# Kernel optimization log

Measured on AMD Instinct MI355X. Metric: run time of the kernel, lower is better.

## Reference

```python
import jax, jax.numpy as jnp
import numpy as np

B, SEG, DIM = 8, 16, 1024  # H = W = D = SEG is forced by the Linear(dim, dim) on H*S etc.
HID = DIM // 4


def setup_inputs() -> dict:
    key = jax.random.key(0)
    ks = jax.random.split(key, 16)
    def lin(k, i, o):
        return jax.random.normal(k, (i, o), jnp.float32) * 0.02
    return {
        "x": jax.random.normal(ks[0], (B, SEG, SEG, SEG, DIM), jnp.float32),
        "wh": lin(ks[1], DIM, DIM), "bh": jnp.zeros((DIM,), jnp.float32),
        "ww": lin(ks[2], DIM, DIM), "bw": jnp.zeros((DIM,), jnp.float32),
        "wd": lin(ks[3], DIM, DIM), "bd": jnp.zeros((DIM,), jnp.float32),
        "wc": lin(ks[4], DIM, DIM), "bc": jnp.zeros((DIM,), jnp.float32),
        "w1": lin(ks[5], DIM, HID), "b1": jnp.zeros((HID,), jnp.float32),
        "w2": lin(ks[6], HID, 4 * DIM), "b2": jnp.zeros((4 * DIM,), jnp.float32),
        "wp": lin(ks[7], DIM, DIM), "bp": jnp.zeros((DIM,), jnp.float32),
    }


def reference(x, wh, bh, ww, bw, wd, bd, wc, bc, w1, b1, w2, b2, wp, bp):
    Bn, H, Wn, D, C = x.shape
    seg = SEG
    S = C // seg
    xr = x.reshape(Bn, H, Wn, D, seg, S)

    # h-branch: mix along H axis (H*S == C)
    h = xr.transpose(0, 4, 2, 3, 1, 5).reshape(Bn, seg, Wn, D, H * S)
    h = (h @ wh + bh).reshape(Bn, seg, Wn, D, H, S).transpose(0, 4, 2, 3, 1, 5).reshape(Bn, H, Wn, D, C)

    # w-branch: mix along W axis
    w = xr.transpose(0, 1, 4, 3, 2, 5).reshape(Bn, H, seg, D, Wn * S)
    w = (w @ ww + bw).reshape(Bn, H, seg, D, Wn, S).transpose(0, 1, 4, 3, 2, 5).reshape(Bn, H, Wn, D, C)

    # d-branch: mix along D axis
    d = xr.transpose(0, 1, 2, 4, 3, 5).reshape(Bn, H, Wn, seg, D * S)
    d = (d @ wd + bd).reshape(Bn, H, Wn, seg, D, S).transpose(0, 1, 2, 4, 3, 5).reshape(Bn, H, Wn, D, C)

    # c-branch: plain channel mixing
    c = x @ wc + bc

    # reweight gate: global-average-pool then small MLP -> softmax over the 4 branches
    a = (h + w + d + c).mean(axis=(1, 2, 3))                 # (B, C)
    a = jax.nn.gelu(a @ w1 + b1, approximate=False) @ w2 + b2  # (B, 4C)
    a = jax.nn.softmax(a.reshape(Bn, C, 4).transpose(2, 0, 1), axis=0)  # (4, B, C)
    a = a[:, :, None, None, None, :]                          # (4, B, 1, 1, 1, C)

    out = h * a[0] + w * a[1] + d * a[2] + c * a[3]
    return out @ wp + bp
```

## Files before the change

### kernel.cpp

```cpp
#include <hip/hip_runtime.h>
#include <cstdint>
#include <cstddef>

typedef unsigned short u16;
typedef __attribute__((ext_vector_type(8))) __bf16 bf16x8;
typedef __attribute__((ext_vector_type(4))) float f32x4;
typedef __attribute__((ext_vector_type(4))) unsigned int u32x4;

__device__ __forceinline__ float bf2f(u16 u){
  union { unsigned int i; float f; } x; x.i = ((unsigned int)u) << 16; return x.f;
}
__device__ __forceinline__ u16 f2bf(float f){
  union { float f; unsigned int i; } x; x.f = f;
  unsigned int i = x.i;
  return (u16)((i + 0x7fffu + ((i >> 16) & 1u)) >> 16);
}
__device__ __forceinline__ void load_lds16(const u16* g, u16* l){
  __builtin_amdgcn_global_load_lds((const __attribute__((address_space(1))) void*)g,
                                   (__attribute__((address_space(3))) void*)l, 16, 0, 0);
}

__global__ __launch_bounds__(256) void k_transpose(
    const float* __restrict__ wh, const float* __restrict__ ww,
    const float* __restrict__ wd, const float* __restrict__ wc,
    const float* __restrict__ wp, u16* __restrict__ wT)
{
  __shared__ u16 tile[32][33];
  const float* src = (blockIdx.z==0)?wh:(blockIdx.z==1)?ww:(blockIdx.z==2)?wd:(blockIdx.z==3)?wc:wp;
  u16* dst = wT + (size_t)blockIdx.z * 1048576;
  int x = blockIdx.x*32 + threadIdx.x;
  int y0 = blockIdx.y*32;
  for (int i = threadIdx.y; i < 32; i += 8)
    tile[i][threadIdx.x] = f2bf(src[(size_t)(y0+i)*1024 + x]);
  __syncthreads();
  int x2 = y0 + threadIdx.x;
  int y2 = blockIdx.x*32;
  for (int i = threadIdx.y; i < 32; i += 8)
    dst[(size_t)(y2+i)*1024 + x2] = tile[threadIdx.x][i];
}

__global__ __launch_bounds__(256) void k_cast(const float* __restrict__ x, u16* __restrict__ xbf)
{
  size_t i = (size_t)blockIdx.x*256 + threadIdx.x;
  const f32x4* p = (const f32x4*)(x + i*8);
  f32x4 a = p[0], b = p[1];
  union { u32x4 v; u16 u[8]; } o;
#pragma unroll
  for (int e = 0; e < 4; ++e){ o.u[e] = f2bf(a[e]); o.u[e+4] = f2bf(b[e]); }
  *(u32x4*)(xbf + i*8) = o.v;
}

__global__ __launch_bounds__(256) void k_psum(
    const float* __restrict__ x, float* __restrict__ P_h,
    float* __restrict__ PwP, float* __restrict__ PdP)
{
  const int b = blockIdx.x, cs = blockIdx.y, hg = blockIdx.z;
  const int th = threadIdx.x >> 7, tc = threadIdx.x & 127;
  const int h = hg*2 + th, c = cs*128 + tc;
  const float* xb = x + ((size_t)b<<22) + ((size_t)h<<18) + c;
  float sh = 0.f;
  float aW[16] = {}, aD[16] = {};
#pragma unroll
  for (int w = 0; w < 16; ++w)
#pragma unroll
    for (int d = 0; d < 16; ++d){
      float v = xb[(w<<14) + (d<<10)];
      sh += v; aW[w] += v; aD[d] += v;
    }
  P_h[(size_t)((b<<4)+h)*1024 + c] = sh;
  const int part = hg*2 + th;
  float* pw = PwP + ((size_t)part<<17) + ((size_t)b<<14) + c;
  float* pd = PdP + ((size_t)part<<17) + ((size_t)b<<14) + c;
#pragma unroll
  for (int w = 0; w < 16; ++w) pw[w<<10] = aW[w];
#pragma unroll
  for (int d = 0; d < 16; ++d) pd[d<<10] = aD[d];
}

__global__ __launch_bounds__(256) void k_psum2(
    const float* __restrict__ PwP, const float* __restrict__ PdP,
    float* __restrict__ P_w, float* __restrict__ P_d)
{
  int idx = blockIdx.x*256 + threadIdx.x;
  float s = 0.f, t = 0.f;
#pragma unroll
  for (int p = 0; p < 16; ++p){ s += PwP[(size_t)p*131072 + idx]; t += PdP[(size_t)p*131072 + idx]; }
  P_w[idx] = s; P_d[idx] = t;
}

__global__ __launch_bounds__(256) void k_wred(
    const float* __restrict__ wh, const float* __restrict__ ww, const float* __restrict__ wd,
    float* __restrict__ wred)
{
  const float* src = (blockIdx.y==0)?wh:(blockIdx.y==1)?ww:wd;
  int idx = blockIdx.x*256 + threadIdx.x;
  int k = idx >> 6, S = idx & 63;
  float s = 0.f;
#pragma unroll
  for (int i = 0; i < 16; ++i) s += src[(size_t)k*1024 + i*64 + S];
  wred[(size_t)blockIdx.y*65536 + idx] = s;
}

__global__ __launch_bounds__(128) void k_asum(
    const float* __restrict__ P_h, const float* __restrict__ P_w, const float* __restrict__ P_d,
    const float* __restrict__ wred, const float* __restrict__ wc,
    const float* __restrict__ bhv, const float* __restrict__ bwv,
    const float* __restrict__ bdv, const float* __restrict__ bcv,
    float* __restrict__ a_sum)
{
  const int b = blockIdx.x, cs = blockIdx.y, tid = threadIdx.x;
  const int c = cs*128 + tid, sg = c >> 6, S = c & 63;
  __shared__ float xbar[1024];
  for (int k = tid; k < 1024; k += 128){
    float s = 0.f;
#pragma unroll
    for (int hh = 0; hh < 16; ++hh) s += P_h[(size_t)(b*16+hh)*1024 + k];
    xbar[k] = s;
  }
  __syncthreads();
  const float* Ph = P_h + (size_t)b*16384;
  const float* Pw = P_w + (size_t)b*16384;
  const float* Pd = P_d + (size_t)b*16384;
  const float* whr = wred, *wwr = wred + 65536, *wdr = wred + 131072;
  float bs = 0.f;
#pragma unroll
  for (int i = 0; i < 16; ++i) bs += bhv[i*64+S] + bwv[i*64+S] + bdv[i*64+S];
  float acc = 4096.f * bcv[c] + 256.f * bs;
  for (int i = 0; i < 16; ++i){
#pragma unroll 8
    for (int si = 0; si < 64; ++si){
      int k = i*64 + si;
      acc += Ph[i*1024 + sg*64 + si] * whr[(size_t)k*64 + S]
           + Pw[i*1024 + sg*64 + si] * wwr[(size_t)k*64 + S]
           + Pd[i*1024 + sg*64 + si] * wdr[(size_t)k*64 + S];
    }
  }
#pragma unroll 8
  for (int k = 0; k < 1024; ++k) acc += xbar[k] * wc[(size_t)k*1024 + c];
  a_sum[b*1024 + c] = acc;
}

__global__ __launch_bounds__(256) void k_mlp1(
    const float* __restrict__ a_sum, const float* __restrict__ w1,
    const float* __restrict__ b1, float* __restrict__ z1g)
{
  const int b = blockIdx.x, tid = threadIdx.x;
  __shared__ float af[1024];
  for (int i = tid; i < 1024; i += 256) af[i] = a_sum[b*1024 + i] * (1.0f/4096.0f);
  __syncthreads();
  float acc = b1[tid];
#pragma unroll 8
  for (int k = 0; k < 1024; ++k) acc += af[k] * w1[(size_t)k*256 + tid];
  z1g[b*256 + tid] = 0.5f * acc * (1.0f + erff(acc * 0.70710678118654752f));
}

__global__ __launch_bounds__(128) void k_mlp2(
    const float* __restrict__ z1g, const float* __restrict__ w2,
    const float* __restrict__ b2, float* __restrict__ alpha)
{
  const int b = blockIdx.x, js = blockIdx.y, tid = threadIdx.x;
  __shared__ float z1[256];
  z1[tid] = z1g[b*256 + tid];
  z1[tid+128] = z1g[b*256 + tid + 128];
  __syncthreads();
  const int cch = js*128 + tid;
  const int j0 = cch*4;
  f32x4 acc = *(const f32x4*)(b2 + j0);
#pragma unroll 8
  for (int k = 0; k < 256; ++k){
    f32x4 wv4 = *(const f32x4*)(w2 + (size_t)k*4096 + j0);
    float z = z1[k];
    acc[0] += z*wv4[0]; acc[1] += z*wv4[1]; acc[2] += z*wv4[2]; acc[3] += z*wv4[3];
  }
  float m = fmaxf(fmaxf(acc[0], acc[1]), fmaxf(acc[2], acc[3]));
  float e0 = expf(acc[0]-m), e1 = expf(acc[1]-m), e2 = expf(acc[2]-m), e3 = expf(acc[3]-m);
  float inv = 1.0f / (e0+e1+e2+e3);
  alpha[0*8192 + b*1024 + cch] = e0*inv;
  alpha[1*8192 + b*1024 + cch] = e1*inv;
  alpha[2*8192 + b*1024 + cch] = e2*inv;
  alpha[3*8192 + b*1024 + cch] = e3*inv;
}

__global__ __launch_bounds__(256) void k_branch_gemm(
    const u16* __restrict__ xbf, const u16* __restrict__ wT,
    const float* __restrict__ bh, const float* __restrict__ bw,
    const float* __restrict__ bd, const float* __restrict__ bc,
    u16* __restrict__ hbuf, u16* __restrict__ wbuf,
    u16* __restrict__ dbuf, u16* __restrict__ cbuf)
{
  const int branch = blockIdx.z;
  const int ntile  = blockIdx.x;
  const int rtile  = blockIdx.y;
  const int tid = threadIdx.x;
  const int wv = tid >> 6, l = tid & 63;

  __shared__ __align__(16) u16 As[4096];
  __shared__ __align__(16) u16 Bs[4096];

  const u16* wsel = wT + (size_t)branch * 1048576;
  const float* bias = (branch==0)?bh:(branch==1)?bw:(branch==2)?bd:bc;
  u16* obuf         = (branch==0)?hbuf:(branch==1)?wbuf:(branch==2)?dbuf:cbuf;

  const int srow0 = wv*32 + (l>>2);
  const int kelem = (l & 3) * 8;
  size_t basea0, basea1; int strideK;
  {
    int r  = rtile*128 + srow0;
    int r2 = r + 16;
    int b0=r>>12,  q1=(r>>8)&15,  q2=(r>>4)&15,  q3=r&15;
    int b1_=r2>>12, p1=(r2>>8)&15, p2=(r2>>4)&15, p3=r2&15;
    if      (branch==0){ basea0=((size_t)b0<<22)+(q2<<14)+(q3<<10)+(q1<<6);
                         basea1=((size_t)b1_<<22)+(p2<<14)+(p3<<10)+(p1<<6); strideK=262144; }
    else if (branch==1){ basea0=((size_t)b0<<22)+((size_t)q1<<18)+(q3<<10)+(q2<<6);
                         basea1=((size_t)b1_<<22)+((size_t)p1<<18)+(p3<<10)+(p2<<6); strideK=16384; }
    else if (branch==2){ basea0=((size_t)b0<<22)+((size_t)q1<<18)+(q2<<14)+(q3<<6);
                         basea1=((size_t)b1_<<22)+((size_t)p1<<18)+(p2<<14)+(p3<<6); strideK=1024; }
    else               { basea0=(size_t)r<<10; basea1=(size_t)r2<<10; strideK=64; }
  }
  const u16* ga0 = xbf + basea0 + kelem;
  const u16* ga1 = xbf + basea1 + kelem;
  const u16* bp0 = wsel + (size_t)(ntile*128 + srow0)*1024 + kelem;
  const u16* bp1 = bp0 + 16*1024;
  u16* lA0 = As + wv*1024;        u16* lA1 = As + wv*1024 + 512;
  u16* lB0 = Bs + wv*1024;        u16* lB1 = Bs + wv*1024 + 512;

  const int wm = wv >> 1, wn = wv & 1;
  const int fr = l & 15, fq = (l >> 4) * 8;
  const u16* ard = As + (wm*64 + fr)*32 + fq;
  const u16* brd = Bs + (wn*64 + fr)*32 + fq;
  f32x4 acc[4][4] = {};

  for (int s = 0; s < 32; ++s){
    size_t koff = (size_t)(s>>1)*strideK + (size_t)(s&1)*32;
    load_lds16(ga0 + koff, lA0);
    load_lds16(ga1 + koff, lA1);
    load_lds16(bp0 + s*32, lB0);
    load_lds16(bp1 + s*32, lB1);
    __syncthreads();
    bf16x8 af[4], bf[4];
#pragma unroll
    for (int i = 0; i < 4; ++i){
      af[i] = *(const bf16x8*)(ard + i*16*32);
      bf[i] = *(const bf16x8*)(brd + i*16*32);
    }
#pragma unroll
    for (int mf = 0; mf < 4; ++mf)
#pragma unroll
      for (int nf = 0; nf < 4; ++nf)
        acc[mf][nf] = __builtin_amdgcn_mfma_f32_16x16x32_bf16(af[mf], bf[nf], acc[mf][nf], 0, 0, 0);
    __syncthreads();
  }

#pragma unroll
  for (int mf = 0; mf < 4; ++mf)
#pragma unroll
    for (int nf = 0; nf < 4; ++nf){
      int col = ntile*128 + wn*64 + nf*16 + fr;
      float bv = bias[col];
      int row0 = rtile*128 + wm*64 + mf*16 + (l>>4)*4;
#pragma unroll
      for (int rg = 0; rg < 4; ++rg)
        obuf[(size_t)(row0+rg)*1024 + col] = f2bf(acc[mf][nf][rg] + bv);
    }
}

__global__ __launch_bounds__(256) void k_mix(
    const u16* __restrict__ hbuf, const u16* __restrict__ wbuf,
    const u16* __restrict__ dbuf, const u16* __restrict__ cbuf,
    u16* __restrict__ mix, const float* __restrict__ alpha)
{
  int idx = blockIdx.x*256 + threadIdx.x;
  int p  = idx >> 7;
  int c0 = (idx & 127) << 3;
  int b = p >> 12, h = (p >> 8) & 15, w = (p >> 4) & 15, d = p & 15;
  int sg = c0 >> 6, s = c0 & 63;
  size_t bb = (size_t)b << 22;
  union { u32x4 v; u16 u[8]; } hv, wv, dv, cv, mv;
  hv.v = *(const u32x4*)(hbuf + bb + (sg<<18) + (w<<14) + (d<<10) + (h<<6) + s);
  wv.v = *(const u32x4*)(wbuf + bb + (h<<18) + (sg<<14) + (d<<10) + (w<<6) + s);
  dv.v = *(const u32x4*)(dbuf + bb + (h<<18) + (w<<14) + (sg<<10) + (d<<6) + s);
  cv.v = *(const u32x4*)(cbuf + ((size_t)p<<10) + c0);
  union { f32x4 f[2]; float a[8]; } a0, a1, a2, a3;
  const float* ab = alpha + b*1024 + c0;
  a0.f[0] = *(const f32x4*)(ab);         a0.f[1] = *(const f32x4*)(ab + 4);
  a1.f[0] = *(const f32x4*)(ab + 8192);  a1.f[1] = *(const f32x4*)(ab + 8196);
  a2.f[0] = *(const f32x4*)(ab + 16384); a2.f[1] = *(const f32x4*)(ab + 16388);
  a3.f[0] = *(const f32x4*)(ab + 24576); a3.f[1] = *(const f32x4*)(ab + 24580);
#pragma unroll
  for (int e = 0; e < 8; ++e){
    float m = a0.a[e]*bf2f(hv.u[e]) + a1.a[e]*bf2f(wv.u[e])
            + a2.a[e]*bf2f(dv.u[e]) + a3.a[e]*bf2f(cv.u[e]);
    mv.u[e] = f2bf(m);
  }
  *(u32x4*)(mix + ((size_t)p<<10) + c0) = mv.v;
}

__global__ __launch_bounds__(256) void k_final_gemm(
    const u16* __restrict__ A, const u16* __restrict__ wpT,
    const float* __restrict__ bp, float* __restrict__ out)
{
  const int ntile = blockIdx.x, rtile = blockIdx.y;
  const int tid = threadIdx.x;
  const int wv = tid >> 6, l = tid & 63;
  __shared__ __align__(16) u16 As[4096];
  __shared__ __align__(16) u16 Bs[4096];
  const int srow0 = wv*32 + (l>>2);
  const int kelem = (l & 3) * 8;
  const u16* ga0 = A + ((size_t)(rtile*128 + srow0) << 10) + kelem;
  const u16* ga1 = ga0 + (16 << 10);
  const u16* bp0 = wpT + (size_t)(ntile*128 + srow0)*1024 + kelem;
  const u16* bp1 = bp0 + 16*1024;
  u16* lA0 = As + wv*1024;        u16* lA1 = As + wv*1024 + 512;
  u16* lB0 = Bs + wv*1024;        u16* lB1 = Bs + wv*1024 + 512;
  const int wm = wv >> 1, wn = wv & 1;
  const int fr = l & 15, fq = (l >> 4) * 8;
  const u16* ard = As + (wm*64 + fr)*32 + fq;
  const u16* brd = Bs + (wn*64 + fr)*32 + fq;
  f32x4 acc[4][4] = {};

  for (int s = 0; s < 32; ++s){
    load_lds16(ga0 + s*32, lA0);
    load_lds16(ga1 + s*32, lA1);
    load_lds16(bp0 + s*32, lB0);
    load_lds16(bp1 + s*32, lB1);
    __syncthreads();
    bf16x8 af[4], bf[4];
#pragma unroll
    for (int i = 0; i < 4; ++i){
      af[i] = *(const bf16x8*)(ard + i*16*32);
      bf[i] = *(const bf16x8*)(brd + i*16*32);
    }
#pragma unroll
    for (int mf = 0; mf < 4; ++mf)
#pragma unroll
      for (int nf = 0; nf < 4; ++nf)
        acc[mf][nf] = __builtin_amdgcn_mfma_f32_16x16x32_bf16(af[mf], bf[nf], acc[mf][nf], 0, 0, 0);
    __syncthreads();
  }

#pragma unroll
  for (int mf = 0; mf < 4; ++mf)
#pragma unroll
    for (int nf = 0; nf < 4; ++nf){
      int col = ntile*128 + wn*64 + nf*16 + fr;
      float bv = bp[col];
      int row0 = rtile*128 + wm*64 + mf*16 + (l>>4)*4;
#pragma unroll
      for (int rg = 0; rg < 4; ++rg)
        out[(size_t)(row0+rg)*1024 + col] = acc[mf][nf][rg] + bv;
    }
}

extern "C" void kernel_launch(void* const* d_in, const int* in_sizes, int n_in,
                              void* d_out, int out_size, void* d_ws, size_t ws_size,
                              hipStream_t stream)
{
  const float* x  = (const float*)d_in[0];
  const float* wh = (const float*)d_in[1];
  const float* bh = (const float*)d_in[2];
  const float* ww = (const float*)d_in[3];
  const float* bw = (const float*)d_in[4];
  const float* wd = (const float*)d_in[5];
  const float* bd = (const float*)d_in[6];
  const float* wc = (const float*)d_in[7];
  const float* bc = (const float*)d_in[8];
  const float* w1 = (const float*)d_in[9];
  const float* b1 = (const float*)d_in[10];
  const float* w2 = (const float*)d_in[11];
  const float* b2 = (const float*)d_in[12];
  const float* wp = (const float*)d_in[13];
  const float* bp = (const float*)d_in[14];
  char* ws = (char*)d_ws;
  char* ob = (char*)d_out;

  u16*   xbf   = (u16*)(ws);
  u16*   hbuf  = (u16*)(ws + 67108864);
  u16*   wbuf  = (u16*)(ws + 134217728);
  u16*   wT    = (u16*)(ws + 201326592);
  float* a_sum = (float*)(ws + 211812352);
  float* alpha = (float*)(ws + 211845120);
  float* z1g   = (float*)(ws + 211976192);
  u16*   mixb  = xbf;

  float* PwP  = (float*)(ob);
  float* PdP  = (float*)(ob + 8388608);
  float* P_h  = (float*)(ob + 16777216);
  float* P_w  = (float*)(ob + 17301504);
  float* P_d  = (float*)(ob + 17825792);
  float* wred = (float*)(ob + 18350080);
  u16*   cbuf = (u16*)ob;
  u16*   dbuf = (u16*)(ob + 67108864);
  float* outp = (float*)d_out;

  k_transpose  <<<dim3(32, 32, 5), dim3(32, 8), 0, stream>>>(wh, ww, wd, wc, wp, wT);
  k_cast       <<<dim3(16384),     256, 0, stream>>>(x, xbf);
  k_psum       <<<dim3(8, 8, 8),   256, 0, stream>>>(x, P_h, PwP, PdP);
  k_psum2      <<<dim3(512),       256, 0, stream>>>(PwP, PdP, P_w, P_d);
  k_wred       <<<dim3(256, 3),    256, 0, stream>>>(wh, ww, wd, wred);
  k_asum       <<<dim3(8, 8),      128, 0, stream>>>(P_h, P_w, P_d, wred, wc, bh, bw, bd, bc, a_sum);
  k_mlp1       <<<dim3(8),         256, 0, stream>>>(a_sum, w1, b1, z1g);
  k_mlp2       <<<dim3(8, 8),      128, 0, stream>>>(z1g, w2, b2, alpha);
  k_branch_gemm<<<dim3(8, 256, 4), 256, 0, stream>>>(xbf, wT, bh, bw, bd, bc,
                                                     hbuf, wbuf, dbuf, cbuf);
  k_mix        <<<dim3(16384),     256, 0, stream>>>(hbuf, wbuf, dbuf, cbuf, mixb, alpha);
  k_final_gemm <<<dim3(8, 256),    256, 0, stream>>>(mixb, wT + 4*1048576, bp, outp);
  (void)in_sizes; (void)n_in; (void)out_size; (void)ws_size;
}
```

Before: 1.062 ms.

## Rewrite GEMMs as 256x256 pipelined tiles and fuse bf16 cast into psum

Both GEMM kernels now use 512-thread blocks computing 256x256 tiles. They use double-buffered LDS staging through direct global-to-LDS loads, an 8-phase interleaved schedule with explicit waitcnt, barriers and setprio, and an XCD-aware block-index swizzle. The goal is to hide load latency and raise MFMA utilisation. Separately, the standalone cast kernel is removed and the bf16 conversion is done inside k_psum, saving one full read of x. k_asum also splits its reduction across 256 threads for more parallelism. The larger tiles raise register and LDS pressure (128 KB of LDS per block).

```diff
diff --git a/kernel.cpp b/kernel.cpp
--- a/kernel.cpp
+++ b/kernel.cpp
@@ -39,25 +39,16 @@
     dst[(size_t)(y2+i)*1024 + x2] = tile[threadIdx.x][i];
 }
 
-__global__ __launch_bounds__(256) void k_cast(const float* __restrict__ x, u16* __restrict__ xbf)
-{
-  size_t i = (size_t)blockIdx.x*256 + threadIdx.x;
-  const f32x4* p = (const f32x4*)(x + i*8);
-  f32x4 a = p[0], b = p[1];
-  union { u32x4 v; u16 u[8]; } o;
-#pragma unroll
-  for (int e = 0; e < 4; ++e){ o.u[e] = f2bf(a[e]); o.u[e+4] = f2bf(b[e]); }
-  *(u32x4*)(xbf + i*8) = o.v;
-}
-
 __global__ __launch_bounds__(256) void k_psum(
-    const float* __restrict__ x, float* __restrict__ P_h,
+    const float* __restrict__ x, u16* __restrict__ xbf, float* __restrict__ P_h,
     float* __restrict__ PwP, float* __restrict__ PdP)
 {
   const int b = blockIdx.x, cs = blockIdx.y, hg = blockIdx.z;
   const int th = threadIdx.x >> 7, tc = threadIdx.x & 127;
   const int h = hg*2 + th, c = cs*128 + tc;
-  const float* xb = x + ((size_t)b<<22) + ((size_t)h<<18) + c;
+  const size_t base = ((size_t)b<<22) + ((size_t)h<<18) + c;
+  const float* xb = x + base;
+  u16* xo = xbf + base;
   float sh = 0.f;
   float aW[16] = {}, aD[16] = {};
 #pragma unroll
@@ -65,6 +56,7 @@
 #pragma unroll
     for (int d = 0; d < 16; ++d){
       float v = xb[(w<<14) + (d<<10)];
+      xo[(w<<14) + (d<<10)] = f2bf(v);
       sh += v; aW[w] += v; aD[d] += v;
     }
   P_h[(size_t)((b<<4)+h)*1024 + c] = sh;
@@ -101,7 +93,7 @@
   wred[(size_t)blockIdx.y*65536 + idx] = s;
 }
 
-__global__ __launch_bounds__(128) void k_asum(
+__global__ __launch_bounds__(256) void k_asum(
     const float* __restrict__ P_h, const float* __restrict__ P_w, const float* __restrict__ P_d,
     const float* __restrict__ wred, const float* __restrict__ wc,
     const float* __restrict__ bhv, const float* __restrict__ bwv,
@@ -109,9 +101,11 @@
     float* __restrict__ a_sum)
 {
   const int b = blockIdx.x, cs = blockIdx.y, tid = threadIdx.x;
-  const int c = cs*128 + tid, sg = c >> 6, S = c & 63;
+  const int tc = tid & 127, ti = tid >> 7;
+  const int c = cs*128 + tc, sg = c >> 6, S = c & 63;
   __shared__ float xbar[1024];
-  for (int k = tid; k < 1024; k += 128){
+  __shared__ float red[2][128];
+  for (int k = tid; k < 1024; k += 256){
     float s = 0.f;
 #pragma unroll
     for (int hh = 0; hh < 16; ++hh) s += P_h[(size_t)(b*16+hh)*1024 + k];
@@ -122,11 +116,8 @@
   const float* Pw = P_w + (size_t)b*16384;
   const float* Pd = P_d + (size_t)b*16384;
   const float* whr = wred, *wwr = wred + 65536, *wdr = wred + 131072;
-  float bs = 0.f;
-#pragma unroll
-  for (int i = 0; i < 16; ++i) bs += bhv[i*64+S] + bwv[i*64+S] + bdv[i*64+S];
-  float acc = 4096.f * bcv[c] + 256.f * bs;
-  for (int i = 0; i < 16; ++i){
+  float acc = 0.f;
+  for (int i = ti*8; i < ti*8 + 8; ++i){
 #pragma unroll 8
     for (int si = 0; si < 64; ++si){
       int k = i*64 + si;
@@ -136,8 +127,15 @@
     }
   }
 #pragma unroll 8
-  for (int k = 0; k < 1024; ++k) acc += xbar[k] * wc[(size_t)k*1024 + c];
-  a_sum[b*1024 + c] = acc;
+  for (int k = ti*512; k < ti*512 + 512; ++k) acc += xbar[k] * wc[(size_t)k*1024 + c];
+  red[ti][tc] = acc;
+  __syncthreads();
+  if (ti == 0){
+    float bs = 0.f;
+#pragma unroll
+    for (int i = 0; i < 16; ++i) bs += bhv[i*64+S] + bwv[i*64+S] + bdv[i*64+S];
+    a_sum[b*1024 + c] = red[0][tc] + red[1][tc] + 4096.f*bcv[c] + 256.f*bs;
+  }
 }
 
 __global__ __launch_bounds__(256) void k_mlp1(
@@ -181,86 +179,134 @@
   alpha[3*8192 + b*1024 + cch] = e3*inv;
 }
 
-__global__ __launch_bounds__(256) void k_branch_gemm(
+
+#define STAGE_A(buf, kk, kt) \
+  load_lds16(gA0 + (size_t)(kt)*strideK + (kk)*32, sA + (buf)*16384 + (kk)*8192); \
+  load_lds16(gA1 + (size_t)(kt)*strideK + (kk)*32, sA + (buf)*16384 + (kk)*8192 + 4096)
+#define STAGE_B(buf, kk, kt) \
+  load_lds16(gB0 + (kt)*64 + (kk)*32, sB + (buf)*16384 + (kk)*8192); \
+  load_lds16(gB1 + (kt)*64 + (kk)*32, sB + (buf)*16384 + (kk)*8192 + 4096)
+
+#define PHASE(h, kk, buf, STAGE_STMT, VM) do{ \
+  const u16* ar_ = ldsA + (buf)*16384 + (kk)*8192 + ardoff + (h)*2048; \
+  const u16* br_ = ldsB + (buf)*16384 + (kk)*8192 + brdoff; \
+  bf16x8 af_[4], bf_[4]; \
+  _Pragma("unroll") for (int m_ = 0; m_ < 4; ++m_) af_[m_] = *(const bf16x8*)(ar_ + m_*512); \
+  _Pragma("unroll") for (int n_ = 0; n_ < 4; ++n_) bf_[n_] = *(const bf16x8*)(br_ + n_*512); \
+  STAGE_STMT; \
+  if (VM) asm volatile("s_waitcnt vmcnt(4)" ::: "memory"); \
+  __builtin_amdgcn_s_barrier(); \
+  asm volatile("s_waitcnt lgkmcnt(0)" ::: "memory"); \
+  __builtin_amdgcn_sched_barrier(0); \
+  __builtin_amdgcn_s_setprio(1); \
+  _Pragma("unroll") for (int m_ = 0; m_ < 4; ++m_) \
+    _Pragma("unroll") for (int n_ = 0; n_ < 4; ++n_) \
+      acc[(h)*4+m_][n_] = __builtin_amdgcn_mfma_f32_16x16x32_bf16(af_[m_], bf_[n_], acc[(h)*4+m_][n_], 0, 0, 0); \
+  __builtin_amdgcn_s_setprio(0); \
+  __builtin_amdgcn_s_barrier(); \
+}while(0)
+
+#define GEMM_PROLOGUE() do{ \
+  load_lds16(gA0, sA);                 load_lds16(gA1, sA + 4096); \
+  load_lds16(gB0, sB);                 load_lds16(gB1, sB + 4096); \
+  load_lds16(gA0 + 32, sA + 8192);     load_lds16(gA1 + 32, sA + 8192 + 4096); \
+  load_lds16(gB0 + 32, sB + 8192);     load_lds16(gB1 + 32, sB + 8192 + 4096); \
+  load_lds16(gA0 + strideK, sA + 16384);   load_lds16(gA1 + strideK, sA + 16384 + 4096); \
+  load_lds16(gB0 + 64, sB + 16384);        load_lds16(gB1 + 64, sB + 16384 + 4096); \
+  asm volatile("s_waitcnt vmcnt(4)" ::: "memory"); \
+  __builtin_amdgcn_s_barrier(); \
+}while(0)
+
+#define GEMM_MAINLOOP() \
+  for (int i = 0; i < 8; ++i){ \
+    const int t1 = 2*i + 1; \
+    const int t2 = (2*i + 2 < 16) ? 2*i + 2 : 15; \
+    const int t3 = (2*i + 3 < 16) ? 2*i + 3 : 15; \
+    PHASE(0,0,0, STAGE_A(1,1,t1), 0); \
+    PHASE(1,0,0, STAGE_B(1,1,t1), 0); \
+    PHASE(0,1,0, STAGE_A(0,0,t2), 0); \
+    PHASE(1,1,0, STAGE_B(0,0,t2), 1); \
+    PHASE(0,0,1, STAGE_A(0,1,t2), 0); \
+    PHASE(1,0,1, STAGE_B(0,1,t2), 0); \
+    PHASE(0,1,1, STAGE_A(1,0,t3), 0); \
+    PHASE(1,1,1, STAGE_B(1,0,t3), 1); \
+  }
+
+__global__ __launch_bounds__(512, 2) void k_branch_gemm(
     const u16* __restrict__ xbf, const u16* __restrict__ wT,
     const float* __restrict__ bh, const float* __restrict__ bw,
     const float* __restrict__ bd, const float* __restrict__ bc,
     u16* __restrict__ hbuf, u16* __restrict__ wbuf,
     u16* __restrict__ dbuf, u16* __restrict__ cbuf)
 {
-  const int branch = blockIdx.z;
-  const int ntile  = blockIdx.x;
-  const int rtile  = blockIdx.y;
+  const int p = blockIdx.x;
+  const int id = (p & 7) * 256 + (p >> 3);
+  const int ntile  = id & 3;
+  const int rtile  = (id >> 2) & 127;
+  const int branch = id >> 9;
+
   const int tid = threadIdx.x;
   const int wv = tid >> 6, l = tid & 63;
 
-  __shared__ __align__(16) u16 As[4096];
-  __shared__ __align__(16) u16 Bs[4096];
+  __shared__ __align__(16) u16 ldsA[32768];
+  __shared__ __align__(16) u16 ldsB[32768];
 
   const u16* wsel = wT + (size_t)branch * 1048576;
   const float* bias = (branch==0)?bh:(branch==1)?bw:(branch==2)?bd:bc;
   u16* obuf         = (branch==0)?hbuf:(branch==1)?wbuf:(branch==2)?dbuf:cbuf;
 
-  const int srow0 = wv*32 + (l>>2);
-  const int kelem = (l & 3) * 8;
-  size_t basea0, basea1; int strideK;
+  const int lr = l >> 2;
+  const int qg = (l & 3) * 8;
+  int strideK;
+  size_t cb0, cb1;
   {
-    int r  = rtile*128 + srow0;
-    int r2 = r + 16;
-    int b0=r>>12,  q1=(r>>8)&15,  q2=(r>>4)&15,  q3=r&15;
-    int b1_=r2>>12, p1=(r2>>8)&15, p2=(r2>>4)&15, p3=r2&15;
-    if      (branch==0){ basea0=((size_t)b0<<22)+(q2<<14)+(q3<<10)+(q1<<6);
-                         basea1=((size_t)b1_<<22)+(p2<<14)+(p3<<10)+(p1<<6); strideK=262144; }
-    else if (branch==1){ basea0=((size_t)b0<<22)+((size_t)q1<<18)+(q3<<10)+(q2<<6);
-                         basea1=((size_t)b1_<<22)+((size_t)p1<<18)+(p3<<10)+(p2<<6); strideK=16384; }
-    else if (branch==2){ basea0=((size_t)b0<<22)+((size_t)q1<<18)+(q2<<14)+(q3<<6);
-                         basea1=((size_t)b1_<<22)+((size_t)p1<<18)+(p2<<14)+(p3<<6); strideK=1024; }
-    else               { basea0=(size_t)r<<10; basea1=(size_t)r2<<10; strideK=64; }
-  }
-  const u16* ga0 = xbf + basea0 + kelem;
-  const u16* ga1 = xbf + basea1 + kelem;
-  const u16* bp0 = wsel + (size_t)(ntile*128 + srow0)*1024 + kelem;
-  const u16* bp1 = bp0 + 16*1024;
-  u16* lA0 = As + wv*1024;        u16* lA1 = As + wv*1024 + 512;
-  u16* lB0 = Bs + wv*1024;        u16* lB1 = Bs + wv*1024 + 512;
-
-  const int wm = wv >> 1, wn = wv & 1;
-  const int fr = l & 15, fq = (l >> 4) * 8;
-  const u16* ard = As + (wm*64 + fr)*32 + fq;
-  const u16* brd = Bs + (wn*64 + fr)*32 + fq;
-  f32x4 acc[4][4] = {};
-
-  for (int s = 0; s < 32; ++s){
-    size_t koff = (size_t)(s>>1)*strideK + (size_t)(s&1)*32;
-    load_lds16(ga0 + koff, lA0);
-    load_lds16(ga1 + koff, lA1);
-    load_lds16(bp0 + s*32, lB0);
-    load_lds16(bp1 + s*32, lB1);
-    __syncthreads();
-    bf16x8 af[4], bf[4];
-#pragma unroll
-    for (int i = 0; i < 4; ++i){
-      af[i] = *(const bf16x8*)(ard + i*16*32);
-      bf[i] = *(const bf16x8*)(brd + i*16*32);
+    const int q1 = rtile & 15, b_ = rtile >> 4;
+    const size_t q2a = wv, q2b = wv + 8;
+    if (branch == 0){
+      cb0 = ((size_t)b_<<22) + (q2a<<14) + ((size_t)q1<<6);
+      cb1 = ((size_t)b_<<22) + (q2b<<14) + ((size_t)q1<<6);
+      strideK = 262144;
+    } else if (branch == 1){
+      cb0 = ((size_t)b_<<22) + ((size_t)q1<<18) + (q2a<<6);
+      cb1 = ((size_t)b_<<22) + ((size_t)q1<<18) + (q2b<<6);
+      strideK = 16384;
+    } else if (branch == 2){
+      cb0 = ((size_t)b_<<22) + ((size_t)q1<<18) + (q2a<<14);
+      cb1 = ((size_t)b_<<22) + ((size_t)q1<<18) + (q2b<<14);
+      strideK = 1024;
+    } else {
+      size_t r0 = (size_t)(rtile*256 + wv*16);
+      cb0 = r0 << 10; cb1 = (r0 + 128) << 10;
+      strideK = 64;
     }
-#pragma unroll
-    for (int mf = 0; mf < 4; ++mf)
-#pragma unroll
-      for (int nf = 0; nf < 4; ++nf)
-        acc[mf][nf] = __builtin_amdgcn_mfma_f32_16x16x32_bf16(af[mf], bf[nf], acc[mf][nf], 0, 0, 0);
-    __syncthreads();
-  }
-
-#pragma unroll
-  for (int mf = 0; mf < 4; ++mf)
+  }
+  const int rsh = (branch == 2) ? 6 : 10;
+  const u16* gA0 = xbf + cb0 + ((size_t)lr << rsh) + qg;
+  const u16* gA1 = xbf + cb1 + ((size_t)lr << rsh) + qg;
+  const u16* gB0 = wsel + (size_t)(ntile*256 + wv*16 + lr) * 1024 + qg;
+  const u16* gB1 = gB0 + 128*1024;
+  u16* sA = ldsA + wv*512;
+  u16* sB = ldsB + wv*512;
+
+  const int wm = wv >> 2, wn = wv & 3;
+  const int fr = l & 15;
+  const int ardoff = (wm*128 + fr)*32 + (l >> 4)*8;
+  const int brdoff = (wn*64  + fr)*32 + (l >> 4)*8;
+  f32x4 acc[8][4] = {};
+
+  GEMM_PROLOGUE();
+  GEMM_MAINLOOP();
+
+#pragma unroll
+  for (int mg = 0; mg < 8; ++mg)
 #pragma unroll
     for (int nf = 0; nf < 4; ++nf){
-      int col = ntile*128 + wn*64 + nf*16 + fr;
+      int col = ntile*256 + wn*64 + nf*16 + fr;
       float bv = bias[col];
-      int row0 = rtile*128 + wm*64 + mf*16 + (l>>4)*4;
+      int row0 = rtile*256 + wm*128 + mg*16 + (l>>4)*4;
 #pragma unroll
       for (int rg = 0; rg < 4; ++rg)
-        obuf[(size_t)(row0+rg)*1024 + col] = f2bf(acc[mf][nf][rg] + bv);
+        obuf[(size_t)(row0+rg)*1024 + col] = f2bf(acc[mg][nf][rg] + bv);
     }
 }
 
@@ -295,59 +341,51 @@
   *(u32x4*)(mix + ((size_t)p<<10) + c0) = mv.v;
 }
 
-__global__ __launch_bounds__(256) void k_final_gemm(
+__global__ __launch_bounds__(512, 2) void k_final_gemm(
     const u16* __restrict__ A, const u16* __restrict__ wpT,
     const float* __restrict__ bp, float* __restrict__ out)
 {
-  const int ntile = blockIdx.x, rtile = blockIdx.y;
+  const int p = blockIdx.x;
+  const int id = (p & 7) * 64 + (p >> 3);
+  const int ntile = id & 3;
+  const int rtile = id >> 2;
+
   const int tid = threadIdx.x;
   const int wv = tid >> 6, l = tid & 63;
-  __shared__ __align__(16) u16 As[4096];
-  __shared__ __align__(16) u16 Bs[4096];
-  const int srow0 = wv*32 + (l>>2);
-  const int kelem = (l & 3) * 8;
-  const u16* ga0 = A + ((size_t)(rtile*128 + srow0) << 10) + kelem;
-  const u16* ga1 = ga0 + (16 << 10);
-  const u16* bp0 = wpT + (size_t)(ntile*128 + srow0)*1024 + kelem;
-  const u16* bp1 = bp0 + 16*1024;
-  u16* lA0 = As + wv*1024;        u16* lA1 = As + wv*1024 + 512;
-  u16* lB0 = Bs + wv*1024;        u16* lB1 = Bs + wv*1024 + 512;
-  const int wm = wv >> 1, wn = wv & 1;
-  const int fr = l & 15, fq = (l >> 4) * 8;
-  const u16* ard = As + (wm*64 + fr)*32 + fq;
-  const u16* brd = Bs + (wn*64 + fr)*32 + fq;
-  f32x4 acc[4][4] = {};
-
-  for (int s = 0; s < 32; ++s){
-    load_lds16(ga0 + s*32, lA0);
-    load_lds16(ga1 + s*32, lA1);
-    load_lds16(bp0 + s*32, lB0);
-    load_lds16(bp1 + s*32, lB1);
-    __syncthreads();
-    bf16x8 af[4], bf[4];
-#pragma unroll
-    for (int i = 0; i < 4; ++i){
-      af[i] = *(const bf16x8*)(ard + i*16*32);
-      bf[i] = *(const bf16x8*)(brd + i*16*32);
-    }
-#pragma unroll
-    for (int mf = 0; mf < 4; ++mf)
-#pragma unroll
-      for (int nf = 0; nf < 4; ++nf)
-        acc[mf][nf] = __builtin_amdgcn_mfma_f32_16x16x32_bf16(af[mf], bf[nf], acc[mf][nf], 0, 0, 0);
-    __syncthreads();
-  }
-
-#pragma unroll
-  for (int mf = 0; mf < 4; ++mf)
+
+  __shared__ __align__(16) u16 ldsA[32768];
+  __shared__ __align__(16) u16 ldsB[32768];
+
+  const int lr = l >> 2;
+  const int qg = (l & 3) * 8;
+  const int strideK = 64;
+  const size_t r0 = (size_t)(rtile*256 + wv*16);
+  const u16* gA0 = A + (r0 << 10) + ((size_t)lr << 10) + qg;
+  const u16* gA1 = A + ((r0 + 128) << 10) + ((size_t)lr << 10) + qg;
+  const u16* gB0 = wpT + (size_t)(ntile*256 + wv*16 + lr) * 1024 + qg;
+  const u16* gB1 = gB0 + 128*1024;
+  u16* sA = ldsA + wv*512;
+  u16* sB = ldsB + wv*512;
+
+  const int wm = wv >> 2, wn = wv & 3;
+  const int fr = l & 15;
+  const int ardoff = (wm*128 + fr)*32 + (l >> 4)*8;
+  const int brdoff = (wn*64  + fr)*32 + (l >> 4)*8;
+  f32x4 acc[8][4] = {};
+
+  GEMM_PROLOGUE();
+  GEMM_MAINLOOP();
+
+#pragma unroll
+  for (int mg = 0; mg < 8; ++mg)
 #pragma unroll
     for (int nf = 0; nf < 4; ++nf){
-      int col = ntile*128 + wn*64 + nf*16 + fr;
+      int col = ntile*256 + wn*64 + nf*16 + fr;
       float bv = bp[col];
-      int row0 = rtile*128 + wm*64 + mf*16 + (l>>4)*4;
+      int row0 = rtile*256 + wm*128 + mg*16 + (l>>4)*4;
 #pragma unroll
       for (int rg = 0; rg < 4; ++rg)
-        out[(size_t)(row0+rg)*1024 + col] = acc[mf][nf][rg] + bv;
+        out[(size_t)(row0+rg)*1024 + col] = acc[mg][nf][rg] + bv;
     }
 }
 
@@ -393,16 +431,15 @@
   float* outp = (float*)d_out;
 
   k_transpose  <<<dim3(32, 32, 5), dim3(32, 8), 0, stream>>>(wh, ww, wd, wc, wp, wT);
-  k_cast       <<<dim3(16384),     256, 0, stream>>>(x, xbf);
-  k_psum       <<<dim3(8, 8, 8),   256, 0, stream>>>(x, P_h, PwP, PdP);
+  k_psum       <<<dim3(8, 8, 8),   256, 0, stream>>>(x, xbf, P_h, PwP, PdP);
   k_psum2      <<<dim3(512),       256, 0, stream>>>(PwP, PdP, P_w, P_d);
   k_wred       <<<dim3(256, 3),    256, 0, stream>>>(wh, ww, wd, wred);
-  k_asum       <<<dim3(8, 8),      128, 0, stream>>>(P_h, P_w, P_d, wred, wc, bh, bw, bd, bc, a_sum);
+  k_asum       <<<dim3(8, 8),      256, 0, stream>>>(P_h, P_w, P_d, wred, wc, bh, bw, bd, bc, a_sum);
   k_mlp1       <<<dim3(8),         256, 0, stream>>>(a_sum, w1, b1, z1g);
   k_mlp2       <<<dim3(8, 8),      128, 0, stream>>>(z1g, w2, b2, alpha);
-  k_branch_gemm<<<dim3(8, 256, 4), 256, 0, stream>>>(xbf, wT, bh, bw, bd, bc,
+  k_branch_gemm<<<dim3(2048),      512, 0, stream>>>(xbf, wT, bh, bw, bd, bc,
                                                      hbuf, wbuf, dbuf, cbuf);
   k_mix        <<<dim3(16384),     256, 0, stream>>>(hbuf, wbuf, dbuf, cbuf, mixb, alpha);
-  k_final_gemm <<<dim3(8, 256),    256, 0, stream>>>(mixb, wT + 4*1048576, bp, outp);
+  k_final_gemm <<<dim3(512),       512, 0, stream>>>(mixb, wT + 4*1048576, bp, outp);
   (void)in_sizes; (void)n_in; (void)out_size; (void)ws_size;
 }
```

Result: faster. 968.8 us (-8.8%).
